# Kernel tuning notes

Measured on AMD Instinct MI355X. Metric: run time of the kernel, lower is better.

The kernel has to match this reference:

```python
import jax, jax.numpy as jnp
import numpy as np

# dims: T x B x IN input, weight (H, K, IN), state (B, H, K)
T, B, IN, H, K = 512, 32, 256, 256, 10
GAP = 0.5                      # gap_penalty buffer (not trainable)
ALPHA = (1.0 / 0.5 ** 2) / K   # exp kernel: 1/sigma^2, divided by kmer_size in __init__
EPS = 1e-4


def setup_inputs() -> dict:
    key = jax.random.key(0)
    k1, k2 = jax.random.split(key)
    x = jax.random.normal(k1, (T, B, IN), dtype=jnp.float32)
    stdv = 1.0 / np.sqrt(H)    # reset_parameters: uniform(-1/sqrt(hidden), 1/sqrt(hidden))
    weight = jax.random.uniform(k2, (H, K, IN), dtype=jnp.float32, minval=-stdv, maxval=stdv)
    return {"x": x, "weight": weight}


def _kappa(u):
    # kernels['exp'](x, alpha) = exp(alpha * (x - 1))
    return jnp.exp(ALPHA * (u - 1.0))


def _matrix_inverse_sqrt(m, eps=1e-4):
    # ops.matrix_inverse_sqrt: symmetric eig, clamp eigenvalues, M^{-1/2}
    e, v = jnp.linalg.eigh(m)
    return (v * (1.0 / jnp.sqrt(jnp.clip(e, eps)))) @ v.T


def _forward(x, wn):
    # ---- _conv_layer: per-step RKHS feature map ----
    norm = jnp.linalg.norm(x, axis=-1, keepdims=True)[..., None]      # T,B,1,1
    b = jnp.einsum('tbi,hki->tbhk', x, wn)                            # T,B,H,K
    b = norm * _kappa(b / jnp.clip(norm, EPS))

    # ---- _compute_lintrans: prod over kmer of kappa(gram), then inverse sqrt ----
    gram = _kappa(jnp.einsum('hki,gki->khg', wn, wn))                 # K,H,H
    lin = _matrix_inverse_sqrt(jnp.prod(gram, axis=0))                # H,H (symmetric)

    # ---- gap-penalty recurrence over time (rkn_forward, multiplicative) ----
    # c_t[j] = gap * c_{t-1}[j] + c_{t-1}[j-1] * b_t[j],  c_{t-1}[0-1] := 1
    hx0 = jnp.zeros((B, H, K), dtype=x.dtype)
    def step(hx, bt):
        prev = jnp.concatenate([jnp.ones_like(hx[..., :1]), hx[..., :-1]], axis=-1)
        hx = GAP * hx + prev * bt
        return hx, hx
    hx_T, cs = jax.lax.scan(step, hx0, b)                             # cs: T,B,H,K

    # ---- mean pooling + select last kmer index + whitening by lintrans ----
    output = cs.mean(axis=0)[..., -1] @ lin                           # B,H (torch.mm)
    outputs = cs[..., -1] @ lin                                       # T,B,H (F.linear; lin symmetric)
    return output, outputs, hx_T


def reference(x, weight):
    # normalize_(weight, dim=-1): unit-norm each (h,k) filter over input dim
    wn = weight / jnp.clip(jnp.linalg.norm(weight, axis=-1, keepdims=True), EPS)
    return _forward(x, wn)
```

## Files before the change

### kernel.cpp

```cpp
#include <hip/hip_runtime.h>
#include <hip/hip_bf16.h>

#define T_DIM 512
#define B_DIM 32
#define IN_DIM 256
#define H_DIM 256
#define K_DIM 10
#define TB 16384
#define NKH 2560
#define NPOW 3

typedef __attribute__((ext_vector_type(8))) short short8;
typedef __attribute__((ext_vector_type(4))) float f32x4;
typedef __attribute__((ext_vector_type(4), aligned(4))) int int4u;

#define GLOBAL_AS __attribute__((address_space(1)))
#define LDS_AS __attribute__((address_space(3)))

__device__ __forceinline__ float wave_sum64(float v) {
    #pragma unroll
    for (int off = 32; off > 0; off >>= 1) v += __shfl_xor(v, off, 64);
    return v;
}

__device__ __forceinline__ float bf_lo(int u) { return __int_as_float(u << 16); }
__device__ __forceinline__ float bf_hi(int u) { return __int_as_float(u & 0xffff0000); }

__global__ __launch_bounds__(256) void prep_kernel(const float* __restrict__ w,
        const float* __restrict__ x, __hip_bfloat16* __restrict__ wb,
        __hip_bfloat16* __restrict__ wb2, float* __restrict__ xninfo,
        __hip_bfloat16* __restrict__ xb) {
    int wv = threadIdx.x >> 6, lane = threadIdx.x & 63;
    if (blockIdx.x < 640) {
        int row = blockIdx.x * 4 + wv;
        const float* src = w + (size_t)row * IN_DIM;
        float v[4]; float s = 0.f;
        #pragma unroll
        for (int j = 0; j < 4; ++j) { v[j] = src[lane + 64 * j]; s += v[j] * v[j]; }
        s = wave_sum64(s);
        float inv = 1.f / fmaxf(sqrtf(s), 1e-4f);
        int h = row / K_DIM, k = row % K_DIM;
        __hip_bfloat16* d1 = wb + (size_t)row * IN_DIM;
        __hip_bfloat16* d2 = wb2 + (size_t)h * NKH + k * IN_DIM;
        #pragma unroll
        for (int j = 0; j < 4; ++j) {
            __hip_bfloat16 t = __float2bfloat16(v[j] * inv);
            d1[lane + 64 * j] = t;
            d2[lane + 64 * j] = t;
        }
    } else {
        int row = (blockIdx.x - 640) * 4 + wv;
        const float* src = x + (size_t)row * IN_DIM;
        float v[4]; float s = 0.f;
        #pragma unroll
        for (int j = 0; j < 4; ++j) { v[j] = src[lane + 64 * j]; s += v[j] * v[j]; }
        s = wave_sum64(s);
        float nrm = sqrtf(s);
        if (lane == 0) { xninfo[2 * row] = nrm; xninfo[2 * row + 1] = 1.f / fmaxf(nrm, 1e-4f); }
        __hip_bfloat16* d = xb + (size_t)row * IN_DIM;
        #pragma unroll
        for (int j = 0; j < 4; ++j) d[lane + 64 * j] = __float2bfloat16(v[j]);
    }
}

__global__ __launch_bounds__(256) void gemm_b_mfma(const __hip_bfloat16* __restrict__ xb,
        const __hip_bfloat16* __restrict__ wb, const float* __restrict__ xninfo,
        __hip_bfloat16* __restrict__ bmat) {
    __shared__ __hip_bfloat16 As[2][4096];
    __shared__ __hip_bfloat16 Bs[2][4096];
    int tid = threadIdx.x;
    int wid = tid >> 6, lane = tid & 63;
    int m0 = blockIdx.x * 128, n0 = blockIdx.y * 128;
    int wr = wid >> 1, wc = wid & 1;
    int srow = tid >> 2;
    int scol = (tid & 3) * 8;
    f32x4 acc[4][4] = {};

    const __hip_bfloat16* ga0 = xb + (size_t)(m0 + srow) * IN_DIM + scol;
    const __hip_bfloat16* gb0 = wb + (size_t)(n0 + srow) * IN_DIM + scol;

    #pragma unroll
    for (int half = 0; half < 2; ++half) {
        __builtin_amdgcn_global_load_lds((const GLOBAL_AS void*)(ga0 + half * 64 * IN_DIM),
            (LDS_AS void*)(&As[0][half * 2048 + wid * 512]), 16, 0, 0);
        __builtin_amdgcn_global_load_lds((const GLOBAL_AS void*)(gb0 + half * 64 * IN_DIM),
            (LDS_AS void*)(&Bs[0][half * 2048 + wid * 512]), 16, 0, 0);
    }
    __syncthreads();

    int cur = 0;
    for (int step = 0; step < 8; ++step) {
        if (step < 7) {
            int kbn = (step + 1) * 32;
            #pragma unroll
            for (int half = 0; half < 2; ++half) {
                __builtin_amdgcn_global_load_lds((const GLOBAL_AS void*)(ga0 + half * 64 * IN_DIM + kbn),
                    (LDS_AS void*)(&As[cur ^ 1][half * 2048 + wid * 512]), 16, 0, 0);
                __builtin_amdgcn_global_load_lds((const GLOBAL_AS void*)(gb0 + half * 64 * IN_DIM + kbn),
                    (LDS_AS void*)(&Bs[cur ^ 1][half * 2048 + wid * 512]), 16, 0, 0);
            }
        }
        int seg = (lane >> 4) * 8;
        int rl = lane & 15;
        short8 a[4], b[4];
        #pragma unroll
        for (int m = 0; m < 4; ++m)
            a[m] = *(const short8*)(&As[cur][(wr * 64 + m * 16 + rl) * 32 + seg]);
        #pragma unroll
        for (int n = 0; n < 4; ++n)
            b[n] = *(const short8*)(&Bs[cur][(wc * 64 + n * 16 + rl) * 32 + seg]);
        #pragma unroll
        for (int m = 0; m < 4; ++m)
            #pragma unroll
            for (int n = 0; n < 4; ++n)
                acc[m][n] = __builtin_amdgcn_mfma_f32_16x16x32_bf16(a[m], b[n], acc[m][n], 0, 0, 0);
        __syncthreads();
        cur ^= 1;
    }

    int col_l = lane & 15;
    int rseg = (lane >> 4) * 4;
    #pragma unroll
    for (int m = 0; m < 4; ++m) {
        int rbase = m0 + wr * 64 + m * 16 + rseg;
        float4 q0 = *(const float4*)(xninfo + 2 * rbase);
        float4 q1 = *(const float4*)(xninfo + 2 * rbase + 4);
        float nrm[4] = { q0.x, q0.z, q1.x, q1.z };
        float inv[4] = { q0.y, q0.w, q1.y, q1.w };
        #pragma unroll
        for (int n = 0; n < 4; ++n) {
            int col = n0 + wc * 64 + n * 16 + col_l;
            #pragma unroll
            for (int j = 0; j < 4; ++j) {
                float bv = nrm[j] * __expf(0.4f * acc[m][n][j] * inv[j] - 0.4f);
                bmat[(size_t)(rbase + j) * NKH + col] = __float2bfloat16(bv);
            }
        }
    }
}

__global__ __launch_bounds__(256) void gram_partial(const __hip_bfloat16* __restrict__ wb2,
        float* __restrict__ Mpart) {
    __shared__ __hip_bfloat16 As[2][4096];
    __shared__ __hip_bfloat16 Bs[2][4096];
    int tid = threadIdx.x;
    int wid = tid >> 6, lane = tid & 63;
    int m0 = blockIdx.x * 128, n0 = blockIdx.y * 128;
    int kz = blockIdx.z;
    int wr = wid >> 1, wc = wid & 1;
    int srow = tid >> 2;
    int scol = (tid & 3) * 8;
    f32x4 acc[4][4] = {};

    const __hip_bfloat16* ga0 = wb2 + (size_t)(m0 + srow) * NKH + kz * 160 + scol;
    const __hip_bfloat16* gb0 = wb2 + (size_t)(n0 + srow) * NKH + kz * 160 + scol;

    #pragma unroll
    for (int half = 0; half < 2; ++half) {
        __builtin_amdgcn_global_load_lds((const GLOBAL_AS void*)(ga0 + half * 64 * NKH),
            (LDS_AS void*)(&As[0][half * 2048 + wid * 512]), 16, 0, 0);
        __builtin_amdgcn_global_load_lds((const GLOBAL_AS void*)(gb0 + half * 64 * NKH),
            (LDS_AS void*)(&Bs[0][half * 2048 + wid * 512]), 16, 0, 0);
    }
    __syncthreads();

    int cur = 0;
    for (int ks = 0; ks < 5; ++ks) {
        if (ks < 4) {
            int kbn = (ks + 1) * 32;
            #pragma unroll
            for (int half = 0; half < 2; ++half) {
                __builtin_amdgcn_global_load_lds((const GLOBAL_AS void*)(ga0 + half * 64 * NKH + kbn),
                    (LDS_AS void*)(&As[cur ^ 1][half * 2048 + wid * 512]), 16, 0, 0);
                __builtin_amdgcn_global_load_lds((const GLOBAL_AS void*)(gb0 + half * 64 * NKH + kbn),
                    (LDS_AS void*)(&Bs[cur ^ 1][half * 2048 + wid * 512]), 16, 0, 0);
            }
        }
        int seg = (lane >> 4) * 8;
        int rl = lane & 15;
        short8 a[4], b[4];
        #pragma unroll
        for (int m = 0; m < 4; ++m)
            a[m] = *(const short8*)(&As[cur][(wr * 64 + m * 16 + rl) * 32 + seg]);
        #pragma unroll
        for (int n = 0; n < 4; ++n)
            b[n] = *(const short8*)(&Bs[cur][(wc * 64 + n * 16 + rl) * 32 + seg]);
        #pragma unroll
        for (int m = 0; m < 4; ++m)
            #pragma unroll
            for (int n = 0; n < 4; ++n)
                acc[m][n] = __builtin_amdgcn_mfma_f32_16x16x32_bf16(a[m], b[n], acc[m][n], 0, 0, 0);
        __syncthreads();
        cur ^= 1;
    }

    float* dst = Mpart + (size_t)kz * 65536;
    int col_l = lane & 15;
    int rseg = (lane >> 4) * 4;
    #pragma unroll
    for (int m = 0; m < 4; ++m) {
        int rbase = m0 + wr * 64 + m * 16 + rseg;
        #pragma unroll
        for (int n = 0; n < 4; ++n) {
            int col = n0 + wc * 64 + n * 16 + col_l;
            #pragma unroll
            for (int j = 0; j < 4; ++j)
                dst[(size_t)(rbase + j) * H_DIM + col] = acc[m][n][j];
        }
    }
}

__global__ __launch_bounds__(256) void gram_finish(const float* __restrict__ Mpart,
        float* __restrict__ Mm, float* __restrict__ rsum) {
    __shared__ float red[256];
    int r = blockIdx.x, c = threadIdx.x;
    float s = 0.f;
    #pragma unroll
    for (int kz = 0; kz < 16; ++kz)
        s += Mpart[(size_t)kz * 65536 + (size_t)r * H_DIM + c];
    float e = __expf(0.4f * s - 4.0f);
    Mm[(size_t)r * H_DIM + c] = e;
    red[c] = e;
    __syncthreads();
    #pragma unroll
    for (int st = 128; st > 0; st >>= 1) {
        if (c < st) red[c] += red[c + st];
        __syncthreads();
    }
    if (c == 0) rsum[r] = red[0];
}

__device__ __forceinline__ float power_phase(const float* __restrict__ Mm,
        const float* __restrict__ rsum, float* vv, float* red, int tid) {
    vv[tid] = rsum[tid];
    __syncthreads();
    float lam = 0.f;
    for (int it = 0; it <= NPOW; ++it) {
        float p = 0.f;
        #pragma unroll 8
        for (int g = 0; g < 256; ++g) p = fmaf(Mm[(size_t)g * 256 + tid], vv[g], p);
        __syncthreads();
        if (it < NPOW) {
            red[tid] = p * p;
            __syncthreads();
            #pragma unroll
            for (int st = 128; st > 0; st >>= 1) {
                if (tid < st) red[tid] += red[tid + st];
                __syncthreads();
            }
            float inv = rsqrtf(red[0]);
            __syncthreads();
            vv[tid] = p * inv;
            __syncthreads();
        } else {
            red[tid] = p * vv[tid];
            __syncthreads();
            #pragma unroll
            for (int st = 128; st > 0; st >>= 1) {
                if (tid < st) red[tid] += red[tid + st];
                __syncthreads();
            }
            lam = red[0];
            __syncthreads();
        }
    }
    return lam;
}

__global__ __launch_bounds__(256) void e2_kernel(const float* __restrict__ Mm,
        const float* __restrict__ rsum, float* __restrict__ E2g,
        __hip_bfloat16* __restrict__ e2b) {
    __shared__ __hip_bfloat16 EA[16384];
    __shared__ __hip_bfloat16 EC[16384];
    __shared__ float vv[256];
    __shared__ float redl[256];
    int tid = threadIdx.x;
    int r0 = (blockIdx.x >> 2) * 64, c0 = (blockIdx.x & 3) * 64;
    float lam = power_phase(Mm, rsum, vv, redl, tid);
    float lm1 = lam - 1.f;
    char* pa = (char*)EA;
    char* pc = (char*)EC;
    for (int f = tid; f < 4096; f += 256) {
        int row = f >> 6, c4 = (f & 63) << 2;
        {
            int r = r0 + row;
            float4 mv = *(const float4*)(Mm + (size_t)r * 256 + c4);
            float vr = lm1 * vv[r];
            __hip_bfloat16 hb[4];
            hb[0] = __float2bfloat16(mv.x - ((r == c4 + 0) ? 1.f : 0.f) - vr * vv[c4 + 0]);
            hb[1] = __float2bfloat16(mv.y - ((r == c4 + 1) ? 1.f : 0.f) - vr * vv[c4 + 1]);
            hb[2] = __float2bfloat16(mv.z - ((r == c4 + 2) ? 1.f : 0.f) - vr * vv[c4 + 2]);
            hb[3] = __float2bfloat16(mv.w - ((r == c4 + 3) ? 1.f : 0.f) - vr * vv[c4 + 3]);
            *(short4*)(pa + row * 512 + ((c4 * 2) ^ ((row & 7) << 4))) = *(short4*)hb;
        }
        {
            int r = c0 + row;
            float4 mv = *(const float4*)(Mm + (size_t)r * 256 + c4);
            float vr = lm1 * vv[r];
            __hip_bfloat16 hb[4];
            hb[0] = __float2bfloat16(mv.x - ((r == c4 + 0) ? 1.f : 0.f) - vr * vv[c4 + 0]);
            hb[1] = __float2bfloat16(mv.y - ((r == c4 + 1) ? 1.f : 0.f) - vr * vv[c4 + 1]);
            hb[2] = __float2bfloat16(mv.z - ((r == c4 + 2) ? 1.f : 0.f) - vr * vv[c4 + 2]);
            hb[3] = __float2bfloat16(mv.w - ((r == c4 + 3) ? 1.f : 0.f) - vr * vv[c4 + 3]);
            *(short4*)(pc + row * 512 + ((c4 * 2) ^ ((row & 7) << 4))) = *(short4*)hb;
        }
    }
    __syncthreads();
    int wv = tid >> 6, lane = tid & 63;
    int rl = lane & 15, seg8 = (lane >> 4) * 8;
    f32x4 acc[4] = {};
    for (int kb = 0; kb < 256; kb += 32) {
        int row = wv * 16 + rl;
        short8 a = *(const short8*)(pa + row * 512 + (((kb + seg8) * 2) ^ ((rl & 7) << 4)));
        short8 b[4];
        #pragma unroll
        for (int n = 0; n < 4; ++n) {
            int rowb = n * 16 + rl;
            b[n] = *(const short8*)(pc + rowb * 512 + (((kb + seg8) * 2) ^ ((rl & 7) << 4)));
        }
        #pragma unroll
        for (int n = 0; n < 4; ++n)
            acc[n] = __builtin_amdgcn_mfma_f32_16x16x32_bf16(a, b[n], acc[n], 0, 0, 0);
    }
    int col_l = lane & 15, rseg = (lane >> 4) * 4;
    #pragma unroll
    for (int n = 0; n < 4; ++n) {
        #pragma unroll
        for (int j = 0; j < 4; ++j) {
            int r = r0 + wv * 16 + rseg + j;
            int c = c0 + n * 16 + col_l;
            size_t idx = (size_t)r * 256 + c;
            E2g[idx] = acc[n][j];
            e2b[idx] = __float2bfloat16(acc[n][j]);
        }
    }
}

__global__ __launch_bounds__(256) void e3lin_kernel(const float* __restrict__ Mm,
        const float* __restrict__ rsum, const float* __restrict__ E2g,
        const __hip_bfloat16* __restrict__ e2b,
        float* __restrict__ lin, __hip_bfloat16* __restrict__ linb) {
    __shared__ __hip_bfloat16 EA[16384];
    __shared__ __hip_bfloat16 EC[16384];
    __shared__ float vv[256];
    __shared__ float redl[256];
    int tid = threadIdx.x;
    int r0 = (blockIdx.x >> 2) * 64, c0 = (blockIdx.x & 3) * 64;
    float lam = power_phase(Mm, rsum, vv, redl, tid);
    float lm1 = lam - 1.f;
    float wfac = 0.5f * lm1 + (rsqrtf(lam) - 1.f);
    char* pa = (char*)EA;
    char* pc = (char*)EC;
    for (int f = tid; f < 4096; f += 256) {
        int row = f >> 6, c4 = (f & 63) << 2;
        int r = r0 + row;
        float4 mv = *(const float4*)(Mm + (size_t)r * 256 + c4);
        float vr = lm1 * vv[r];
        __hip_bfloat16 hb[4];
        hb[0] = __float2bfloat16(mv.x - ((r == c4 + 0) ? 1.f : 0.f) - vr * vv[c4 + 0]);
        hb[1] = __float2bfloat16(mv.y - ((r == c4 + 1) ? 1.f : 0.f) - vr * vv[c4 + 1]);
        hb[2] = __float2bfloat16(mv.z - ((r == c4 + 2) ? 1.f : 0.f) - vr * vv[c4 + 2]);
        hb[3] = __float2bfloat16(mv.w - ((r == c4 + 3) ? 1.f : 0.f) - vr * vv[c4 + 3]);
        *(short4*)(pa + row * 512 + ((c4 * 2) ^ ((row & 7) << 4))) = *(short4*)hb;
    }
    for (int f = tid; f < 2048; f += 256) {
        int row = f >> 5, c8 = (f & 31) << 3;
        short8 v8 = *(const short8*)(e2b + (size_t)(c0 + row) * 256 + c8);
        *(short8*)(pc + row * 512 + ((c8 * 2) ^ ((row & 7) << 4))) = v8;
    }
    __syncthreads();
    int wv = tid >> 6, lane = tid & 63;
    int rl = lane & 15, seg8 = (lane >> 4) * 8;
    f32x4 acc[4] = {};
    for (int kb = 0; kb < 256; kb += 32) {
        int row = wv * 16 + rl;
        short8 a = *(const short8*)(pa + row * 512 + (((kb + seg8) * 2) ^ ((rl & 7) << 4)));
        short8 b[4];
        #pragma unroll
        for (int n = 0; n < 4; ++n) {
            int rowb = n * 16 + rl;
            b[n] = *(const short8*)(pc + rowb * 512 + (((kb + seg8) * 2) ^ ((rl & 7) << 4)));
        }
        #pragma unroll
        for (int n = 0; n < 4; ++n)
            acc[n] = __builtin_amdgcn_mfma_f32_16x16x32_bf16(a, b[n], acc[n], 0, 0, 0);
    }
    int col_l = lane & 15, rseg = (lane >> 4) * 4;
    #pragma unroll
    for (int n = 0; n < 4; ++n) {
        #pragma unroll
        for (int j = 0; j < 4; ++j) {
            int r = r0 + wv * 16 + rseg + j;
            int c = c0 + n * 16 + col_l;
            size_t idx = (size_t)r * 256 + c;
            float lv = ((r == c) ? 1.5f : 0.f) - 0.5f * Mm[idx] + wfac * vv[r] * vv[c]
                     + 0.375f * E2g[idx] - 0.3125f * acc[n][j];
            lin[idx] = lv;
            linb[idx] = __float2bfloat16(lv);
        }
    }
}

__global__ __launch_bounds__(256) void megarec(const __hip_bfloat16* __restrict__ bmat,
        const __hip_bfloat16* __restrict__ linb, float* __restrict__ out1,
        float* __restrict__ part, float* __restrict__ hxT) {
    __shared__ __hip_bfloat16 c9t[8192];
    int tid = threadIdx.x;
    int s = blockIdx.x >> 5;
    int b = blockIdx.x & 31;
    int h = tid;
    int tout0 = s * 32;
    int t0 = (s == 0) ? 0 : tout0 - 32;
    int t1 = tout0 + 32;
    char* c9p = (char*)c9t;
    float c[10] = {};
    float s9 = 0.f;
    int4u v0; int v1;
    {
        const char* bp = (const char*)bmat + ((size_t)(t0 * B_DIM + b) * NKH + h * 10) * 2;
        v0 = *(const int4u*)bp;
        v1 = *(const int*)(bp + 16);
    }
    for (int t = t0; t < t1; ++t) {
        int tn = (t + 1 < t1) ? t + 1 : t;
        const char* bq = (const char*)bmat + ((size_t)(tn * B_DIM + b) * NKH + h * 10) * 2;
        int4u w0 = *(const int4u*)bq;
        int w1 = *(const int*)(bq + 16);
        float bt[10];
        bt[0] = bf_lo(v0.x); bt[1] = bf_hi(v0.x);
        bt[2] = bf_lo(v0.y); bt[3] = bf_hi(v0.y);
        bt[4] = bf_lo(v0.z); bt[5] = bf_hi(v0.z);
        bt[6] = bf_lo(v0.w); bt[7] = bf_hi(v0.w);
        bt[8] = bf_lo(v1);   bt[9] = bf_hi(v1);
        #pragma unroll
        for (int j = 9; j >= 1; --j) c[j] = 0.5f * c[j] + c[j - 1] * bt[j];
        c[0] = 0.5f * c[0] + bt[0];
        if (t >= tout0) {
            int tt = t - tout0;
            *(__hip_bfloat16*)(c9p + tt * 512 + ((h * 2) ^ ((tt & 7) << 4))) = __float2bfloat16(c[9]);
            s9 += c[9];
        }
        v0 = w0; v1 = w1;
    }
    part[(size_t)(s * B_DIM + b) * H_DIM + h] = s9;
    if (s == 15) {
        float* hp = hxT + (size_t)(b * H_DIM + h) * K_DIM;
        #pragma unroll
        for (int k = 0; k < 10; ++k) hp[k] = c[k];
    }
    __syncthreads();
    int wid = tid >> 6, lane = tid & 63;
    int rl = lane & 15, seg8 = (lane >> 4) * 8;
    int col_l = lane & 15, rseg = (lane >> 4) * 4;
    f32x4 acc[2][4] = {};
    for (int kb = 0; kb < 256; kb += 32) {
        short8 a[2];
        #pragma unroll
        for (int m = 0; m < 2; ++m) {
            int row = m * 16 + rl;
            a[m] = *(const short8*)(c9p + row * 512 + (((kb + seg8) * 2) ^ ((row & 7) << 4)));
        }
        short8 bf[4];
        #pragma unroll
        for (int n = 0; n < 4; ++n)
            bf[n] = *(const short8*)(linb + (size_t)(wid * 64 + n * 16 + rl) * 256 + kb + seg8);
        #pragma unroll
        for (int m = 0; m < 2; ++m)
            #pragma unroll
            for (int n = 0; n < 4; ++n)
                acc[m][n] = __builtin_amdgcn_mfma_f32_16x16x32_bf16(a[m], bf[n], acc[m][n], 0, 0, 0);
    }
    #pragma unroll
    for (int m = 0; m < 2; ++m) {
        #pragma unroll
        for (int n = 0; n < 4; ++n) {
            int g = wid * 64 + n * 16 + col_l;
            #pragma unroll
            for (int j = 0; j < 4; ++j) {
                int tt = m * 16 + rseg + j;
                out1[((size_t)(tout0 + tt) * B_DIM + b) * H_DIM + g] = acc[m][n][j];
            }
        }
    }
}

__global__ __launch_bounds__(256) void recout_kernel(const float* __restrict__ part,
        const float* __restrict__ lin, float* __restrict__ out0) {
    __shared__ float mrow[256];
    int b = blockIdx.x, tid = threadIdx.x;
    float s = 0.f;
    #pragma unroll
    for (int j = 0; j < 16; ++j) s += part[(size_t)(j * B_DIM + b) * H_DIM + tid];
    mrow[tid] = s * (1.f / T_DIM);
    __syncthreads();
    float acc = 0.f;
    #pragma unroll 8
    for (int h = 0; h < H_DIM; ++h) acc = fmaf(mrow[h], lin[(size_t)h * H_DIM + tid], acc);
    out0[b * H_DIM + tid] = acc;
}

extern "C" void kernel_launch(void* const* d_in, const int* in_sizes, int n_in,
                              void* d_out, int out_size, void* d_ws, size_t ws_size,
                              hipStream_t stream) {
    const float* x = (const float*)d_in[0];
    const float* w = (const float*)d_in[1];
    float* out0 = (float*)d_out;
    float* out1 = out0 + (size_t)B_DIM * H_DIM;
    float* hxT  = out1 + (size_t)TB * H_DIM;

    char* ws = (char*)d_ws;
    __hip_bfloat16* wb   = (__hip_bfloat16*)(ws + 0);
    __hip_bfloat16* wb2  = (__hip_bfloat16*)(ws + 1310720);
    float* xninfo        = (float*)(ws + 2621440);
    float* Mm            = (float*)(ws + 2752512);
    float* rsum          = (float*)(ws + 3014656);
    float* E2g           = (float*)(ws + 3015680);
    __hip_bfloat16* e2b  = (__hip_bfloat16*)(ws + 3277824);
    float* lin           = (float*)(ws + 3408896);
    __hip_bfloat16* linb = (__hip_bfloat16*)(ws + 3671040);
    float* part          = (float*)(ws + 3802112);
    float* Mpart         = (float*)(ws + 4326400);
    __hip_bfloat16* xb   = (__hip_bfloat16*)(ws + 8520704);
    __hip_bfloat16* bmat = (__hip_bfloat16*)(ws + 16909312);

    prep_kernel<<<dim3(4736), dim3(256), 0, stream>>>(w, x, wb, wb2, xninfo, xb);
    gemm_b_mfma<<<dim3(128, 20), dim3(256), 0, stream>>>(xb, wb, xninfo, bmat);
    gram_partial<<<dim3(2, 2, 16), dim3(256), 0, stream>>>(wb2, Mpart);
    gram_finish<<<dim3(256), dim3(256), 0, stream>>>(Mpart, Mm, rsum);
    e2_kernel<<<dim3(16), dim3(256), 0, stream>>>(Mm, rsum, E2g, e2b);
    e3lin_kernel<<<dim3(16), dim3(256), 0, stream>>>(Mm, rsum, E2g, e2b, lin, linb);
    megarec<<<dim3(512), dim3(256), 0, stream>>>(bmat, linb, out1, part, hxT);
    recout_kernel<<<dim3(32), dim3(256), 0, stream>>>(part, lin, out0);
}
```

Baseline: 163.4 us.

## Merge b-GEMM and gram partial GEMM into one launch with 256x128 tiles

Fuses the feature-map GEMM and the gram partial-product GEMM into a single kernel launch, with block index ranges selecting the role. Blocks grow to 512 threads with 256x128 output tiles, so each B tile loaded into LDS is reused across twice as many rows. The aim is to remove one launch gap and let the small gram work overlap with the large GEMM. In exchange, LDS use per block rises and there are fewer, larger blocks, which may lower occupancy.

```diff
diff --git a/kernel.cpp b/kernel.cpp
--- a/kernel.cpp
+++ b/kernel.cpp
@@ -63,149 +63,131 @@
     }
 }
 
-__global__ __launch_bounds__(256) void gemm_b_mfma(const __hip_bfloat16* __restrict__ xb,
+__global__ __launch_bounds__(512) void gemm_gram(const __hip_bfloat16* __restrict__ xb,
         const __hip_bfloat16* __restrict__ wb, const float* __restrict__ xninfo,
-        __hip_bfloat16* __restrict__ bmat) {
-    __shared__ __hip_bfloat16 As[2][4096];
+        __hip_bfloat16* __restrict__ bmat, const __hip_bfloat16* __restrict__ wb2,
+        float* __restrict__ Mpart) {
+    __shared__ __hip_bfloat16 As[2][8192];
     __shared__ __hip_bfloat16 Bs[2][4096];
     int tid = threadIdx.x;
     int wid = tid >> 6, lane = tid & 63;
-    int m0 = blockIdx.x * 128, n0 = blockIdx.y * 128;
     int wr = wid >> 1, wc = wid & 1;
-    int srow = tid >> 2;
-    int scol = (tid & 3) * 8;
-    f32x4 acc[4][4] = {};
-
-    const __hip_bfloat16* ga0 = xb + (size_t)(m0 + srow) * IN_DIM + scol;
-    const __hip_bfloat16* gb0 = wb + (size_t)(n0 + srow) * IN_DIM + scol;
-
-    #pragma unroll
-    for (int half = 0; half < 2; ++half) {
-        __builtin_amdgcn_global_load_lds((const GLOBAL_AS void*)(ga0 + half * 64 * IN_DIM),
-            (LDS_AS void*)(&As[0][half * 2048 + wid * 512]), 16, 0, 0);
-        __builtin_amdgcn_global_load_lds((const GLOBAL_AS void*)(gb0 + half * 64 * IN_DIM),
-            (LDS_AS void*)(&Bs[0][half * 2048 + wid * 512]), 16, 0, 0);
-    }
-    __syncthreads();
-
-    int cur = 0;
-    for (int step = 0; step < 8; ++step) {
-        if (step < 7) {
-            int kbn = (step + 1) * 32;
-            #pragma unroll
-            for (int half = 0; half < 2; ++half) {
-                __builtin_amdgcn_global_load_lds((const GLOBAL_AS void*)(ga0 + half * 64 * IN_DIM + kbn),
-                    (LDS_AS void*)(&As[cur ^ 1][half * 2048 + wid * 512]), 16, 0, 0);
-                __builtin_amdgcn_global_load_lds((const GLOBAL_AS void*)(gb0 + half * 64 * IN_DIM + kbn),
-                    (LDS_AS void*)(&Bs[cur ^ 1][half * 2048 + wid * 512]), 16, 0, 0);
-            }
-        }
-        int seg = (lane >> 4) * 8;
-        int rl = lane & 15;
-        short8 a[4], b[4];
-        #pragma unroll
-        for (int m = 0; m < 4; ++m)
-            a[m] = *(const short8*)(&As[cur][(wr * 64 + m * 16 + rl) * 32 + seg]);
-        #pragma unroll
-        for (int n = 0; n < 4; ++n)
-            b[n] = *(const short8*)(&Bs[cur][(wc * 64 + n * 16 + rl) * 32 + seg]);
-        #pragma unroll
-        for (int m = 0; m < 4; ++m)
-            #pragma unroll
-            for (int n = 0; n < 4; ++n)
-                acc[m][n] = __builtin_amdgcn_mfma_f32_16x16x32_bf16(a[m], b[n], acc[m][n], 0, 0, 0);
-        __syncthreads();
-        cur ^= 1;
-    }
-
+    int seg = (lane >> 4) * 8;
+    int rl = lane & 15;
     int col_l = lane & 15;
     int rseg = (lane >> 4) * 4;
-    #pragma unroll
-    for (int m = 0; m < 4; ++m) {
-        int rbase = m0 + wr * 64 + m * 16 + rseg;
-        float4 q0 = *(const float4*)(xninfo + 2 * rbase);
-        float4 q1 = *(const float4*)(xninfo + 2 * rbase + 4);
-        float nrm[4] = { q0.x, q0.z, q1.x, q1.z };
-        float inv[4] = { q0.y, q0.w, q1.y, q1.w };
-        #pragma unroll
-        for (int n = 0; n < 4; ++n) {
-            int col = n0 + wc * 64 + n * 16 + col_l;
-            #pragma unroll
-            for (int j = 0; j < 4; ++j) {
-                float bv = nrm[j] * __expf(0.4f * acc[m][n][j] * inv[j] - 0.4f);
-                bmat[(size_t)(rbase + j) * NKH + col] = __float2bfloat16(bv);
-            }
-        }
-    }
-}
-
-__global__ __launch_bounds__(256) void gram_partial(const __hip_bfloat16* __restrict__ wb2,
-        float* __restrict__ Mpart) {
-    __shared__ __hip_bfloat16 As[2][4096];
-    __shared__ __hip_bfloat16 Bs[2][4096];
-    int tid = threadIdx.x;
-    int wid = tid >> 6, lane = tid & 63;
-    int m0 = blockIdx.x * 128, n0 = blockIdx.y * 128;
-    int kz = blockIdx.z;
-    int wr = wid >> 1, wc = wid & 1;
-    int srow = tid >> 2;
-    int scol = (tid & 3) * 8;
     f32x4 acc[4][4] = {};
 
-    const __hip_bfloat16* ga0 = wb2 + (size_t)(m0 + srow) * NKH + kz * 160 + scol;
-    const __hip_bfloat16* gb0 = wb2 + (size_t)(n0 + srow) * NKH + kz * 160 + scol;
-
-    #pragma unroll
-    for (int half = 0; half < 2; ++half) {
-        __builtin_amdgcn_global_load_lds((const GLOBAL_AS void*)(ga0 + half * 64 * NKH),
-            (LDS_AS void*)(&As[0][half * 2048 + wid * 512]), 16, 0, 0);
-        __builtin_amdgcn_global_load_lds((const GLOBAL_AS void*)(gb0 + half * 64 * NKH),
-            (LDS_AS void*)(&Bs[0][half * 2048 + wid * 512]), 16, 0, 0);
-    }
-    __syncthreads();
-
-    int cur = 0;
-    for (int ks = 0; ks < 5; ++ks) {
-        if (ks < 4) {
-            int kbn = (ks + 1) * 32;
-            #pragma unroll
-            for (int half = 0; half < 2; ++half) {
-                __builtin_amdgcn_global_load_lds((const GLOBAL_AS void*)(ga0 + half * 64 * NKH + kbn),
-                    (LDS_AS void*)(&As[cur ^ 1][half * 2048 + wid * 512]), 16, 0, 0);
-                __builtin_amdgcn_global_load_lds((const GLOBAL_AS void*)(gb0 + half * 64 * NKH + kbn),
-                    (LDS_AS void*)(&Bs[cur ^ 1][half * 2048 + wid * 512]), 16, 0, 0);
-            }
-        }
-        int seg = (lane >> 4) * 8;
-        int rl = lane & 15;
-        short8 a[4], b[4];
-        #pragma unroll
-        for (int m = 0; m < 4; ++m)
-            a[m] = *(const short8*)(&As[cur][(wr * 64 + m * 16 + rl) * 32 + seg]);
-        #pragma unroll
-        for (int n = 0; n < 4; ++n)
-            b[n] = *(const short8*)(&Bs[cur][(wc * 64 + n * 16 + rl) * 32 + seg]);
-        #pragma unroll
-        for (int m = 0; m < 4; ++m)
+    if (blockIdx.x < 1280) {
+        int m0 = (blockIdx.x & 63) * 256, n0 = (blockIdx.x >> 6) * 128;
+        const __hip_bfloat16* ga0 = xb + (size_t)(m0 + (tid >> 2)) * IN_DIM + (tid & 3) * 8;
+        const __hip_bfloat16* gb0 = wb + (size_t)(n0 + (tid >> 2)) * IN_DIM + (tid & 3) * 8;
+
+        __builtin_amdgcn_global_load_lds((const GLOBAL_AS void*)ga0,
+            (LDS_AS void*)(&As[0][tid * 8]), 16, 0, 0);
+        __builtin_amdgcn_global_load_lds((const GLOBAL_AS void*)(ga0 + (size_t)128 * IN_DIM),
+            (LDS_AS void*)(&As[0][4096 + tid * 8]), 16, 0, 0);
+        __builtin_amdgcn_global_load_lds((const GLOBAL_AS void*)gb0,
+            (LDS_AS void*)(&Bs[0][tid * 8]), 16, 0, 0);
+        __syncthreads();
+
+        int cur = 0;
+        for (int step = 0; step < 8; ++step) {
+            if (step < 7) {
+                int kbn = (step + 1) * 32;
+                __builtin_amdgcn_global_load_lds((const GLOBAL_AS void*)(ga0 + kbn),
+                    (LDS_AS void*)(&As[cur ^ 1][tid * 8]), 16, 0, 0);
+                __builtin_amdgcn_global_load_lds((const GLOBAL_AS void*)(ga0 + (size_t)128 * IN_DIM + kbn),
+                    (LDS_AS void*)(&As[cur ^ 1][4096 + tid * 8]), 16, 0, 0);
+                __builtin_amdgcn_global_load_lds((const GLOBAL_AS void*)(gb0 + kbn),
+                    (LDS_AS void*)(&Bs[cur ^ 1][tid * 8]), 16, 0, 0);
+            }
+            short8 a[4], b[4];
+            #pragma unroll
+            for (int m = 0; m < 4; ++m)
+                a[m] = *(const short8*)(&As[cur][(wr * 64 + m * 16 + rl) * 32 + seg]);
             #pragma unroll
             for (int n = 0; n < 4; ++n)
-                acc[m][n] = __builtin_amdgcn_mfma_f32_16x16x32_bf16(a[m], b[n], acc[m][n], 0, 0, 0);
+                b[n] = *(const short8*)(&Bs[cur][(wc * 64 + n * 16 + rl) * 32 + seg]);
+            #pragma unroll
+            for (int m = 0; m < 4; ++m)
+                #pragma unroll
+                for (int n = 0; n < 4; ++n)
+                    acc[m][n] = __builtin_amdgcn_mfma_f32_16x16x32_bf16(a[m], b[n], acc[m][n], 0, 0, 0);
+            __syncthreads();
+            cur ^= 1;
+        }
+
+        #pragma unroll
+        for (int m = 0; m < 4; ++m) {
+            int rbase = m0 + wr * 64 + m * 16 + rseg;
+            float4 q0 = *(const float4*)(xninfo + 2 * rbase);
+            float4 q1 = *(const float4*)(xninfo + 2 * rbase + 4);
+            float nrm[4] = { q0.x, q0.z, q1.x, q1.z };
+            float inv[4] = { q0.y, q0.w, q1.y, q1.w };
+            #pragma unroll
+            for (int n = 0; n < 4; ++n) {
+                int col = n0 + wc * 64 + n * 16 + col_l;
+                #pragma unroll
+                for (int j = 0; j < 4; ++j) {
+                    float bv = nrm[j] * __expf(0.4f * acc[m][n][j] * inv[j] - 0.4f);
+                    bmat[(size_t)(rbase + j) * NKH + col] = __float2bfloat16(bv);
+                }
+            }
+        }
+    } else {
+        int g = blockIdx.x - 1280;
+        int nt = g & 1, kz = g >> 1;
+        int n0 = nt * 128;
+        const __hip_bfloat16* ga0 = wb2 + (size_t)(tid >> 2) * NKH + kz * 160 + (tid & 3) * 8;
+        const __hip_bfloat16* gb0 = wb2 + (size_t)(n0 + (tid >> 2)) * NKH + kz * 160 + (tid & 3) * 8;
+
+        __builtin_amdgcn_global_load_lds((const GLOBAL_AS void*)ga0,
+            (LDS_AS void*)(&As[0][tid * 8]), 16, 0, 0);
+        __builtin_amdgcn_global_load_lds((const GLOBAL_AS void*)(ga0 + (size_t)128 * NKH),
+            (LDS_AS void*)(&As[0][4096 + tid * 8]), 16, 0, 0);
+        __builtin_amdgcn_global_load_lds((const GLOBAL_AS void*)gb0,
+            (LDS_AS void*)(&Bs[0][tid * 8]), 16, 0, 0);
         __syncthreads();
-        cur ^= 1;
-    }
-
-    float* dst = Mpart + (size_t)kz * 65536;
-    int col_l = lane & 15;
-    int rseg = (lane >> 4) * 4;
-    #pragma unroll
-    for (int m = 0; m < 4; ++m) {
-        int rbase = m0 + wr * 64 + m * 16 + rseg;
-        #pragma unroll
-        for (int n = 0; n < 4; ++n) {
-            int col = n0 + wc * 64 + n * 16 + col_l;
-            #pragma unroll
-            for (int j = 0; j < 4; ++j)
-                dst[(size_t)(rbase + j) * H_DIM + col] = acc[m][n][j];
+
+        int cur = 0;
+        for (int ks = 0; ks < 5; ++ks) {
+            if (ks < 4) {
+                int kbn = (ks + 1) * 32;
+                __builtin_amdgcn_global_load_lds((const GLOBAL_AS void*)(ga0 + kbn),
+                    (LDS_AS void*)(&As[cur ^ 1][tid * 8]), 16, 0, 0);
+                __builtin_amdgcn_global_load_lds((const GLOBAL_AS void*)(ga0 + (size_t)128 * NKH + kbn),
+                    (LDS_AS void*)(&As[cur ^ 1][4096 + tid * 8]), 16, 0, 0);
+                __builtin_amdgcn_global_load_lds((const GLOBAL_AS void*)(gb0 + kbn),
+                    (LDS_AS void*)(&Bs[cur ^ 1][tid * 8]), 16, 0, 0);
+            }
+            short8 a[4], b[4];
+            #pragma unroll
+            for (int m = 0; m < 4; ++m)
+                a[m] = *(const short8*)(&As[cur][(wr * 64 + m * 16 + rl) * 32 + seg]);
+            #pragma unroll
+            for (int n = 0; n < 4; ++n)
+                b[n] = *(const short8*)(&Bs[cur][(wc * 64 + n * 16 + rl) * 32 + seg]);
+            #pragma unroll
+            for (int m = 0; m < 4; ++m)
+                #pragma unroll
+                for (int n = 0; n < 4; ++n)
+                    acc[m][n] = __builtin_amdgcn_mfma_f32_16x16x32_bf16(a[m], b[n], acc[m][n], 0, 0, 0);
+            __syncthreads();
+            cur ^= 1;
+        }
+
+        float* dst = Mpart + (size_t)kz * 65536;
+        #pragma unroll
+        for (int m = 0; m < 4; ++m) {
+            int rbase = wr * 64 + m * 16 + rseg;
+            #pragma unroll
+            for (int n = 0; n < 4; ++n) {
+                int col = n0 + wc * 64 + n * 16 + col_l;
+                #pragma unroll
+                for (int j = 0; j < 4; ++j)
+                    dst[(size_t)(rbase + j) * H_DIM + col] = acc[m][n][j];
+            }
         }
     }
 }
@@ -524,8 +506,7 @@
     __hip_bfloat16* bmat = (__hip_bfloat16*)(ws + 16909312);
 
     prep_kernel<<<dim3(4736), dim3(256), 0, stream>>>(w, x, wb, wb2, xninfo, xb);
-    gemm_b_mfma<<<dim3(128, 20), dim3(256), 0, stream>>>(xb, wb, xninfo, bmat);
-    gram_partial<<<dim3(2, 2, 16), dim3(256), 0, stream>>>(wb2, Mpart);
+    gemm_gram<<<dim3(1312), dim3(512), 0, stream>>>(xb, wb, xninfo, bmat, wb2, Mpart);
     gram_finish<<<dim3(256), dim3(256), 0, stream>>>(Mpart, Mm, rsum);
     e2_kernel<<<dim3(16), dim3(256), 0, stream>>>(Mm, rsum, E2g, e2b);
     e3lin_kernel<<<dim3(16), dim3(256), 0, stream>>>(Mm, rsum, E2g, e2b, lin, linb);
```

Result: slower. 168.8 us (+3.3%).

## Merge feature GEMM and gram partial GEMM into one launch with transposed MFMA output

Applied to the files above, without the earlier changes.

Fuses the b-matrix GEMM and the gram partial GEMM into a single kernel whose blocks branch on block index, removing one launch and letting the small gram work fill idle CUs alongside the large GEMM. It also swaps the MFMA operand order so each lane holds four consecutive output columns, allowing vectorized 8-byte bf16 stores and 16-byte float stores instead of scalar strided writes. The risk is a tail where the gram blocks run last, plus slightly more register pressure from the combined kernel.

```diff
diff --git a/kernel.cpp b/kernel.cpp
--- a/kernel.cpp
+++ b/kernel.cpp
@@ -63,149 +63,134 @@
     }
 }
 
-__global__ __launch_bounds__(256) void gemm_b_mfma(const __hip_bfloat16* __restrict__ xb,
+__global__ __launch_bounds__(256) void gemm_gram(const __hip_bfloat16* __restrict__ xb,
         const __hip_bfloat16* __restrict__ wb, const float* __restrict__ xninfo,
-        __hip_bfloat16* __restrict__ bmat) {
-    __shared__ __hip_bfloat16 As[2][4096];
-    __shared__ __hip_bfloat16 Bs[2][4096];
-    int tid = threadIdx.x;
-    int wid = tid >> 6, lane = tid & 63;
-    int m0 = blockIdx.x * 128, n0 = blockIdx.y * 128;
-    int wr = wid >> 1, wc = wid & 1;
-    int srow = tid >> 2;
-    int scol = (tid & 3) * 8;
-    f32x4 acc[4][4] = {};
-
-    const __hip_bfloat16* ga0 = xb + (size_t)(m0 + srow) * IN_DIM + scol;
-    const __hip_bfloat16* gb0 = wb + (size_t)(n0 + srow) * IN_DIM + scol;
-
-    #pragma unroll
-    for (int half = 0; half < 2; ++half) {
-        __builtin_amdgcn_global_load_lds((const GLOBAL_AS void*)(ga0 + half * 64 * IN_DIM),
-            (LDS_AS void*)(&As[0][half * 2048 + wid * 512]), 16, 0, 0);
-        __builtin_amdgcn_global_load_lds((const GLOBAL_AS void*)(gb0 + half * 64 * IN_DIM),
-            (LDS_AS void*)(&Bs[0][half * 2048 + wid * 512]), 16, 0, 0);
-    }
-    __syncthreads();
-
-    int cur = 0;
-    for (int step = 0; step < 8; ++step) {
-        if (step < 7) {
-            int kbn = (step + 1) * 32;
-            #pragma unroll
-            for (int half = 0; half < 2; ++half) {
-                __builtin_amdgcn_global_load_lds((const GLOBAL_AS void*)(ga0 + half * 64 * IN_DIM + kbn),
-                    (LDS_AS void*)(&As[cur ^ 1][half * 2048 + wid * 512]), 16, 0, 0);
-                __builtin_amdgcn_global_load_lds((const GLOBAL_AS void*)(gb0 + half * 64 * IN_DIM + kbn),
-                    (LDS_AS void*)(&Bs[cur ^ 1][half * 2048 + wid * 512]), 16, 0, 0);
-            }
-        }
-        int seg = (lane >> 4) * 8;
-        int rl = lane & 15;
-        short8 a[4], b[4];
-        #pragma unroll
-        for (int m = 0; m < 4; ++m)
-            a[m] = *(const short8*)(&As[cur][(wr * 64 + m * 16 + rl) * 32 + seg]);
-        #pragma unroll
-        for (int n = 0; n < 4; ++n)
-            b[n] = *(const short8*)(&Bs[cur][(wc * 64 + n * 16 + rl) * 32 + seg]);
-        #pragma unroll
-        for (int m = 0; m < 4; ++m)
-            #pragma unroll
-            for (int n = 0; n < 4; ++n)
-                acc[m][n] = __builtin_amdgcn_mfma_f32_16x16x32_bf16(a[m], b[n], acc[m][n], 0, 0, 0);
-        __syncthreads();
-        cur ^= 1;
-    }
-
-    int col_l = lane & 15;
-    int rseg = (lane >> 4) * 4;
-    #pragma unroll
-    for (int m = 0; m < 4; ++m) {
-        int rbase = m0 + wr * 64 + m * 16 + rseg;
-        float4 q0 = *(const float4*)(xninfo + 2 * rbase);
-        float4 q1 = *(const float4*)(xninfo + 2 * rbase + 4);
-        float nrm[4] = { q0.x, q0.z, q1.x, q1.z };
-        float inv[4] = { q0.y, q0.w, q1.y, q1.w };
-        #pragma unroll
-        for (int n = 0; n < 4; ++n) {
-            int col = n0 + wc * 64 + n * 16 + col_l;
-            #pragma unroll
-            for (int j = 0; j < 4; ++j) {
-                float bv = nrm[j] * __expf(0.4f * acc[m][n][j] * inv[j] - 0.4f);
-                bmat[(size_t)(rbase + j) * NKH + col] = __float2bfloat16(bv);
-            }
-        }
-    }
-}
-
-__global__ __launch_bounds__(256) void gram_partial(const __hip_bfloat16* __restrict__ wb2,
+        __hip_bfloat16* __restrict__ bmat, const __hip_bfloat16* __restrict__ wb2,
         float* __restrict__ Mpart) {
     __shared__ __hip_bfloat16 As[2][4096];
     __shared__ __hip_bfloat16 Bs[2][4096];
     int tid = threadIdx.x;
     int wid = tid >> 6, lane = tid & 63;
-    int m0 = blockIdx.x * 128, n0 = blockIdx.y * 128;
-    int kz = blockIdx.z;
     int wr = wid >> 1, wc = wid & 1;
     int srow = tid >> 2;
     int scol = (tid & 3) * 8;
-    f32x4 acc[4][4] = {};
-
-    const __hip_bfloat16* ga0 = wb2 + (size_t)(m0 + srow) * NKH + kz * 160 + scol;
-    const __hip_bfloat16* gb0 = wb2 + (size_t)(n0 + srow) * NKH + kz * 160 + scol;
-
-    #pragma unroll
-    for (int half = 0; half < 2; ++half) {
-        __builtin_amdgcn_global_load_lds((const GLOBAL_AS void*)(ga0 + half * 64 * NKH),
-            (LDS_AS void*)(&As[0][half * 2048 + wid * 512]), 16, 0, 0);
-        __builtin_amdgcn_global_load_lds((const GLOBAL_AS void*)(gb0 + half * 64 * NKH),
-            (LDS_AS void*)(&Bs[0][half * 2048 + wid * 512]), 16, 0, 0);
-    }
-    __syncthreads();
-
-    int cur = 0;
-    for (int ks = 0; ks < 5; ++ks) {
-        if (ks < 4) {
-            int kbn = (ks + 1) * 32;
-            #pragma unroll
-            for (int half = 0; half < 2; ++half) {
-                __builtin_amdgcn_global_load_lds((const GLOBAL_AS void*)(ga0 + half * 64 * NKH + kbn),
-                    (LDS_AS void*)(&As[cur ^ 1][half * 2048 + wid * 512]), 16, 0, 0);
-                __builtin_amdgcn_global_load_lds((const GLOBAL_AS void*)(gb0 + half * 64 * NKH + kbn),
-                    (LDS_AS void*)(&Bs[cur ^ 1][half * 2048 + wid * 512]), 16, 0, 0);
-            }
-        }
-        int seg = (lane >> 4) * 8;
-        int rl = lane & 15;
-        short8 a[4], b[4];
-        #pragma unroll
-        for (int m = 0; m < 4; ++m)
-            a[m] = *(const short8*)(&As[cur][(wr * 64 + m * 16 + rl) * 32 + seg]);
-        #pragma unroll
-        for (int n = 0; n < 4; ++n)
-            b[n] = *(const short8*)(&Bs[cur][(wc * 64 + n * 16 + rl) * 32 + seg]);
-        #pragma unroll
-        for (int m = 0; m < 4; ++m)
-            #pragma unroll
-            for (int n = 0; n < 4; ++n)
-                acc[m][n] = __builtin_amdgcn_mfma_f32_16x16x32_bf16(a[m], b[n], acc[m][n], 0, 0, 0);
-        __syncthreads();
-        cur ^= 1;
-    }
-
-    float* dst = Mpart + (size_t)kz * 65536;
+    int seg = (lane >> 4) * 8;
+    int rl = lane & 15;
     int col_l = lane & 15;
     int rseg = (lane >> 4) * 4;
-    #pragma unroll
-    for (int m = 0; m < 4; ++m) {
-        int rbase = m0 + wr * 64 + m * 16 + rseg;
-        #pragma unroll
-        for (int n = 0; n < 4; ++n) {
-            int col = n0 + wc * 64 + n * 16 + col_l;
-            #pragma unroll
-            for (int j = 0; j < 4; ++j)
-                dst[(size_t)(rbase + j) * H_DIM + col] = acc[m][n][j];
+    f32x4 acc[4][4] = {};
+
+    if (blockIdx.x < 2560) {
+        int m0 = (blockIdx.x & 127) * 128, n0 = (blockIdx.x >> 7) * 128;
+        const __hip_bfloat16* ga0 = xb + (size_t)(m0 + srow) * IN_DIM + scol;
+        const __hip_bfloat16* gb0 = wb + (size_t)(n0 + srow) * IN_DIM + scol;
+
+        #pragma unroll
+        for (int half = 0; half < 2; ++half) {
+            __builtin_amdgcn_global_load_lds((const GLOBAL_AS void*)(ga0 + half * 64 * IN_DIM),
+                (LDS_AS void*)(&As[0][half * 2048 + wid * 512]), 16, 0, 0);
+            __builtin_amdgcn_global_load_lds((const GLOBAL_AS void*)(gb0 + half * 64 * IN_DIM),
+                (LDS_AS void*)(&Bs[0][half * 2048 + wid * 512]), 16, 0, 0);
+        }
+        __syncthreads();
+
+        int cur = 0;
+        for (int step = 0; step < 8; ++step) {
+            if (step < 7) {
+                int kbn = (step + 1) * 32;
+                #pragma unroll
+                for (int half = 0; half < 2; ++half) {
+                    __builtin_amdgcn_global_load_lds((const GLOBAL_AS void*)(ga0 + half * 64 * IN_DIM + kbn),
+                        (LDS_AS void*)(&As[cur ^ 1][half * 2048 + wid * 512]), 16, 0, 0);
+                    __builtin_amdgcn_global_load_lds((const GLOBAL_AS void*)(gb0 + half * 64 * IN_DIM + kbn),
+                        (LDS_AS void*)(&Bs[cur ^ 1][half * 2048 + wid * 512]), 16, 0, 0);
+                }
+            }
+            short8 a[4], b[4];
+            #pragma unroll
+            for (int m = 0; m < 4; ++m)
+                a[m] = *(const short8*)(&As[cur][(wr * 64 + m * 16 + rl) * 32 + seg]);
+            #pragma unroll
+            for (int n = 0; n < 4; ++n)
+                b[n] = *(const short8*)(&Bs[cur][(wc * 64 + n * 16 + rl) * 32 + seg]);
+            #pragma unroll
+            for (int m = 0; m < 4; ++m)
+                #pragma unroll
+                for (int n = 0; n < 4; ++n)
+                    acc[m][n] = __builtin_amdgcn_mfma_f32_16x16x32_bf16(b[n], a[m], acc[m][n], 0, 0, 0);
+            __syncthreads();
+            cur ^= 1;
+        }
+
+        #pragma unroll
+        for (int m = 0; m < 4; ++m) {
+            int mg = m0 + wr * 64 + m * 16 + col_l;
+            float2 xq = *(const float2*)(xninfo + 2 * mg);
+            float nrm = xq.x, inv = xq.y;
+            #pragma unroll
+            for (int n = 0; n < 4; ++n) {
+                int np = n0 + wc * 64 + n * 16 + rseg;
+                __hip_bfloat16 hb[4];
+                #pragma unroll
+                for (int j = 0; j < 4; ++j)
+                    hb[j] = __float2bfloat16(nrm * __expf(0.4f * acc[m][n][j] * inv - 0.4f));
+                *(short4*)((char*)bmat + ((size_t)mg * NKH + np) * 2) = *(short4*)hb;
+            }
+        }
+    } else {
+        int g = blockIdx.x - 2560;
+        int kz = g & 15, mi = (g >> 4) & 1, ni = g >> 5;
+        int m0 = mi * 128, n0 = ni * 128;
+        const __hip_bfloat16* ga0 = wb2 + (size_t)(m0 + srow) * NKH + kz * 160 + scol;
+        const __hip_bfloat16* gb0 = wb2 + (size_t)(n0 + srow) * NKH + kz * 160 + scol;
+
+        #pragma unroll
+        for (int half = 0; half < 2; ++half) {
+            __builtin_amdgcn_global_load_lds((const GLOBAL_AS void*)(ga0 + half * 64 * NKH),
+                (LDS_AS void*)(&As[0][half * 2048 + wid * 512]), 16, 0, 0);
+            __builtin_amdgcn_global_load_lds((const GLOBAL_AS void*)(gb0 + half * 64 * NKH),
+                (LDS_AS void*)(&Bs[0][half * 2048 + wid * 512]), 16, 0, 0);
+        }
+        __syncthreads();
+
+        int cur = 0;
+        for (int ks = 0; ks < 5; ++ks) {
+            if (ks < 4) {
+                int kbn = (ks + 1) * 32;
+                #pragma unroll
+                for (int half = 0; half < 2; ++half) {
+                    __builtin_amdgcn_global_load_lds((const GLOBAL_AS void*)(ga0 + half * 64 * NKH + kbn),
+                        (LDS_AS void*)(&As[cur ^ 1][half * 2048 + wid * 512]), 16, 0, 0);
+                    __builtin_amdgcn_global_load_lds((const GLOBAL_AS void*)(gb0 + half * 64 * NKH + kbn),
+                        (LDS_AS void*)(&Bs[cur ^ 1][half * 2048 + wid * 512]), 16, 0, 0);
+                }
+            }
+            short8 a[4], b[4];
+            #pragma unroll
+            for (int m = 0; m < 4; ++m)
+                a[m] = *(const short8*)(&As[cur][(wr * 64 + m * 16 + rl) * 32 + seg]);
+            #pragma unroll
+            for (int n = 0; n < 4; ++n)
+                b[n] = *(const short8*)(&Bs[cur][(wc * 64 + n * 16 + rl) * 32 + seg]);
+            #pragma unroll
+            for (int m = 0; m < 4; ++m)
+                #pragma unroll
+                for (int n = 0; n < 4; ++n)
+                    acc[m][n] = __builtin_amdgcn_mfma_f32_16x16x32_bf16(b[n], a[m], acc[m][n], 0, 0, 0);
+            __syncthreads();
+            cur ^= 1;
+        }
+
+        float* dst = Mpart + (size_t)kz * 65536;
+        #pragma unroll
+        for (int m = 0; m < 4; ++m) {
+            int mg = m0 + wr * 64 + m * 16 + col_l;
+            #pragma unroll
+            for (int n = 0; n < 4; ++n) {
+                int np = n0 + wc * 64 + n * 16 + rseg;
+                float4 fv = { acc[m][n][0], acc[m][n][1], acc[m][n][2], acc[m][n][3] };
+                *(float4*)(dst + (size_t)mg * H_DIM + np) = fv;
+            }
         }
     }
 }
@@ -524,8 +509,7 @@
     __hip_bfloat16* bmat = (__hip_bfloat16*)(ws + 16909312);
 
     prep_kernel<<<dim3(4736), dim3(256), 0, stream>>>(w, x, wb, wb2, xninfo, xb);
-    gemm_b_mfma<<<dim3(128, 20), dim3(256), 0, stream>>>(xb, wb, xninfo, bmat);
-    gram_partial<<<dim3(2, 2, 16), dim3(256), 0, stream>>>(wb2, Mpart);
+    gemm_gram<<<dim3(2624), dim3(256), 0, stream>>>(xb, wb, xninfo, bmat, wb2, Mpart);
     gram_finish<<<dim3(256), dim3(256), 0, stream>>>(Mpart, Mm, rsum);
     e2_kernel<<<dim3(16), dim3(256), 0, stream>>>(Mm, rsum, E2g, e2b);
     e3lin_kernel<<<dim3(16), dim3(256), 0, stream>>>(Mm, rsum, E2g, e2b, lin, linb);
```

Measured after the change: 166.0 us. About the same (+1.6%).
